# Performance work log

Measured on AMD Instinct MI355X. Metric: run time of the kernel, lower is better.

## Reference

```python
import jax, jax.numpy as jnp
import numpy as np

N, E, FIN, NH, FOUT = 50000, 800000, 128, 4, 16


def setup_inputs() -> dict:
    key = jax.random.key(0)
    ks = jax.random.split(key, 6)
    x = jax.random.normal(ks[0], (N, FIN), dtype=jnp.float32)
    edge_index = jax.random.randint(ks[1], (2, E), 0, N, dtype=jnp.int64)
    w_proj = jax.random.normal(ks[2], (NH * FOUT, FIN), dtype=jnp.float32) * 0.05
    a_src = jax.random.normal(ks[3], (NH, FOUT), dtype=jnp.float32) * 0.1
    a_trg = jax.random.normal(ks[4], (NH, FOUT), dtype=jnp.float32) * 0.1
    w_skip = jax.random.normal(ks[5], (NH * FOUT, FIN), dtype=jnp.float32) * 0.05
    return {"x": x, "edge_index": edge_index, "w_proj": w_proj,
            "a_src": a_src, "a_trg": a_trg, "w_skip": w_skip}


def reference(x, edge_index, w_proj, a_src, a_trg, w_skip):
    # Dropout is identity in eval mode.
    src, trg = edge_index[0], edge_index[1]
    # Project: [N, NH, FOUT]
    proj = (x @ w_proj.T).reshape(N, NH, FOUT)
    # Per-node attention logits: [N, NH]
    s_src = jnp.einsum('nhf,hf->nh', proj, a_src)
    s_trg = jnp.einsum('nhf,hf->nh', proj, a_trg)
    # Lift to edges and score: [E, NH]
    scores = jax.nn.leaky_relu(s_src[src] + s_trg[trg], negative_slope=0.2)
    # Global-max-shifted exp (matches original, which subtracts the global max)
    exp_scores = jnp.exp(scores - jnp.max(scores))
    # Segment-wise softmax denominator over target nodes
    denom = jax.ops.segment_sum(exp_scores, trg, num_segments=N)  # [N, NH]
    attn = exp_scores / (denom[trg] + 1e-16)                      # [E, NH]
    # Weighted aggregation of lifted source features: [N, NH, FOUT]
    weighted = proj[src] * attn[:, :, None]
    agg = jax.ops.segment_sum(weighted, trg, num_segments=N)
    # Skip projection (FOUT != FIN branch) and concat over heads
    out = agg + (x @ w_skip.T).reshape(N, NH, FOUT)
    out = out.reshape(N, NH * FOUT)
    return jax.nn.elu(out)
```

## Files before the change

kernel.cpp:

```cpp
#include <hip/hip_runtime.h>
#include <cstddef>

#define N_NODES 50000
#define N_EDGES 800000
#define FIN     128
#define NH      4
#define FOUT    16
#define COUT    64
#define STRIPS  (N_NODES / 16)
#define SCAN_BLOCKS ((N_NODES + 255) / 256)
#define NB      128
#define CHUNK   (N_EDGES / NB)
#define HW4     (N_NODES / 4)
#define HBYTES  (HW4 * 4)
#define NQ      4
#define BPQ     (NB / NQ)
#define PBLK    ((HW4 + 255) / 256)
#define E4      (N_EDGES / 4)
#define E4B     ((E4 + 255) / 256)

typedef __bf16 bf16x8 __attribute__((ext_vector_type(8)));
typedef float  f32x4  __attribute__((ext_vector_type(4)));

__global__ __launch_bounds__(256) void k0_init(
    const float* __restrict__ wproj, const float* __restrict__ wskip,
    __bf16* __restrict__ wb)
{
    int gid = blockIdx.x * 256 + threadIdx.x;
    if (gid < (128 * FIN) / 4) {
        int row = gid >> 5;
        float4 v = (row < 64) ? reinterpret_cast<const float4*>(wproj)[gid]
                              : reinterpret_cast<const float4*>(wskip)[gid - 2048];
        __bf16* o = wb + (size_t)gid * 4;
        o[0] = (__bf16)v.x; o[1] = (__bf16)v.y;
        o[2] = (__bf16)v.z; o[3] = (__bf16)v.w;
    }
}

__global__ __launch_bounds__(256) void k1_mfma(
    const float* __restrict__ x, const __bf16* __restrict__ wb,
    const float* __restrict__ asrc, const float* __restrict__ atrg,
    __bf16* __restrict__ projb, float* __restrict__ ssrc, float* __restrict__ strg,
    float* __restrict__ outv)
{
    const int lane  = threadIdx.x & 63;
    const int wid   = blockIdx.x * 4 + (threadIdx.x >> 6);
    const int strip = wid >> 1;
    const int half  = wid & 1;
    if (strip >= STRIPS) return;
    const int r = lane & 15;
    const int g = lane >> 4;
    const int row0 = strip * 16;

    bf16x8 bfr[4][4];
    #pragma unroll
    for (int j = 0; j < 4; ++j) {
        const __bf16* wrow = wb + (size_t)(half * 64 + j * 16 + r) * FIN;
        #pragma unroll
        for (int kk = 0; kk < 4; ++kk)
            bfr[j][kk] = *reinterpret_cast<const bf16x8*>(wrow + kk * 32 + g * 8);
    }

    const float* xrow = x + (size_t)(row0 + r) * FIN + g * 8;
    bf16x8 afr[4];
    #pragma unroll
    for (int kk = 0; kk < 4; ++kk) {
        float4 u0 = *reinterpret_cast<const float4*>(xrow + kk * 32);
        float4 u1 = *reinterpret_cast<const float4*>(xrow + kk * 32 + 4);
        bf16x8 a;
        a[0] = (__bf16)u0.x; a[1] = (__bf16)u0.y;
        a[2] = (__bf16)u0.z; a[3] = (__bf16)u0.w;
        a[4] = (__bf16)u1.x; a[5] = (__bf16)u1.y;
        a[6] = (__bf16)u1.z; a[7] = (__bf16)u1.w;
        afr[kk] = a;
    }

    f32x4 acc[4] = {{0.f,0.f,0.f,0.f},{0.f,0.f,0.f,0.f},
                    {0.f,0.f,0.f,0.f},{0.f,0.f,0.f,0.f}};
    #pragma unroll
    for (int kk = 0; kk < 4; ++kk)
        #pragma unroll
        for (int j = 0; j < 4; ++j)
            acc[j] = __builtin_amdgcn_mfma_f32_16x16x32_bf16(
                         afr[kk], bfr[j][kk], acc[j], 0, 0, 0);

    if (!half) {
        #pragma unroll
        for (int j = 0; j < 4; ++j)
            #pragma unroll
            for (int q = 0; q < 4; ++q)
                projb[(size_t)(row0 + g * 4 + q) * COUT + j * 16 + r] =
                    (__bf16)acc[j][q];
        #pragma unroll
        for (int j = 0; j < 4; ++j) {
            const float as = asrc[j * 16 + r];
            const float at = atrg[j * 16 + r];
            #pragma unroll
            for (int q = 0; q < 4; ++q) {
                float ts = acc[j][q] * as;
                float tt = acc[j][q] * at;
                ts += __shfl_xor(ts, 1); ts += __shfl_xor(ts, 2);
                ts += __shfl_xor(ts, 4); ts += __shfl_xor(ts, 8);
                tt += __shfl_xor(tt, 1); tt += __shfl_xor(tt, 2);
                tt += __shfl_xor(tt, 4); tt += __shfl_xor(tt, 8);
                if (r == 0) {
                    int n = row0 + g * 4 + q;
                    ssrc[(size_t)n * NH + j] = ts;
                    strg[(size_t)n * NH + j] = tt;
                }
            }
        }
    } else {
        #pragma unroll
        for (int j = 0; j < 4; ++j)
            #pragma unroll
            for (int q = 0; q < 4; ++q)
                outv[(size_t)(row0 + g * 4 + q) * COUT + j * 16 + r] = acc[j][q];
    }
}

__global__ __launch_bounds__(1024) void k_hist(
    const int* __restrict__ ei, unsigned* __restrict__ histG,
    unsigned char* __restrict__ rank)
{
    extern __shared__ unsigned h[];
    const int t = threadIdx.x;
    for (int i = t; i < HW4; i += 1024) h[i] = 0;
    __syncthreads();
    const int base = blockIdx.x * CHUNK;
    for (int i = t; i < CHUNK; i += 1024) {
        int tg = ei[N_EDGES + base + i];
        int sh = (tg & 3) * 8;
        unsigned old = atomicAdd(&h[tg >> 2], 1u << sh);
        rank[base + i] = (unsigned char)((old >> sh) & 0xffu);
    }
    __syncthreads();
    unsigned* out = histG + (size_t)blockIdx.x * HW4;
    for (int i = t; i < HW4; i += 1024) out[i] = h[i];
}

__global__ __launch_bounds__(256) void k_colscanA(
    const unsigned* __restrict__ histG, unsigned* __restrict__ offG,
    unsigned* __restrict__ partial)
{
    int p = blockIdx.x * 256 + threadIdx.x;
    if (p >= HW4) return;
    int q = blockIdx.y;
    unsigned run = 0;
    #pragma unroll 4
    for (int b = q * BPQ; b < (q + 1) * BPQ; ++b) {
        unsigned v = histG[(size_t)b * HW4 + p];
        offG[(size_t)b * HW4 + p] = run;
        run += v;
    }
    partial[(size_t)q * HW4 + p] = run;
}

__global__ __launch_bounds__(256) void k_scanfuse(
    const unsigned* __restrict__ partial, unsigned* __restrict__ baseQ,
    int* __restrict__ deg, int* __restrict__ tmpExc, int* __restrict__ bsum)
{
    __shared__ int sm[256];
    const int t = threadIdx.x;
    if (t < 64) {
        int p = blockIdx.x * 64 + t;
        if (p < HW4) {
            unsigned s = 0;
            #pragma unroll
            for (int q = 0; q < NQ; ++q) {
                baseQ[(size_t)q * HW4 + p] = s;
                s += partial[(size_t)q * HW4 + p];
            }
            int4 d4 = make_int4((int)(s & 0xffu), (int)((s >> 8) & 0xffu),
                                (int)((s >> 16) & 0xffu), (int)(s >> 24));
            reinterpret_cast<int4*>(deg)[p] = d4;
            sm[4 * t + 0] = d4.x; sm[4 * t + 1] = d4.y;
            sm[4 * t + 2] = d4.z; sm[4 * t + 3] = d4.w;
        } else {
            sm[4 * t + 0] = 0; sm[4 * t + 1] = 0;
            sm[4 * t + 2] = 0; sm[4 * t + 3] = 0;
        }
    }
    __syncthreads();
    int v = sm[t];
    #pragma unroll
    for (int off = 1; off < 256; off <<= 1) {
        int x = (t >= off) ? sm[t - off] : 0;
        __syncthreads();
        sm[t] += x;
        __syncthreads();
    }
    int i = blockIdx.x * 256 + t;
    if (i < N_NODES) tmpExc[i] = sm[t] - v;
    if (t == 255) bsum[blockIdx.x] = sm[t];
}

__global__ __launch_bounds__(256) void scan_b(
    const int* __restrict__ bsum, int* __restrict__ bOff)
{
    __shared__ int sm[256];
    int t = threadIdx.x;
    int v = (t < SCAN_BLOCKS) ? bsum[t] : 0;
    sm[t] = v; __syncthreads();
    #pragma unroll
    for (int off = 1; off < 256; off <<= 1) {
        int x = (t >= off) ? sm[t - off] : 0;
        __syncthreads();
        sm[t] += x;
        __syncthreads();
    }
    if (t < SCAN_BLOCKS) bOff[t] = sm[t] - v;
}

__global__ __launch_bounds__(256) void k_scatter(
    const int* __restrict__ ei, const unsigned char* __restrict__ rank,
    const unsigned* __restrict__ offG, const unsigned* __restrict__ baseQ,
    const int* __restrict__ tmpExc, const int* __restrict__ bOff,
    int* __restrict__ srcs)
{
    int e4 = blockIdx.x * 256 + threadIdx.x;
    if (e4 >= E4) return;
    int4 s4 = reinterpret_cast<const int4*>(ei)[e4];
    int4 t4 = reinterpret_cast<const int4*>(ei + N_EDGES)[e4];
    uchar4 r4 = reinterpret_cast<const uchar4*>(rank)[e4];
    const int e0 = e4 * 4;
    int ss[4] = {s4.x, s4.y, s4.z, s4.w};
    int tt[4] = {t4.x, t4.y, t4.z, t4.w};
    int rr[4] = {r4.x, r4.y, r4.z, r4.w};
    #pragma unroll
    for (int u = 0; u < 4; ++u) {
        int tg = tt[u];
        int b  = (e0 + u) / CHUNK;
        int sh = (tg & 3) * 8;
        unsigned cw = offG[(size_t)b * HW4 + (tg >> 2)]
                    + baseQ[(size_t)(b / BPQ) * HW4 + (tg >> 2)];
        int cross = (int)((cw >> sh) & 0xffu);
        int slot  = tmpExc[tg] + bOff[tg >> 8] + cross + rr[u];
        srcs[slot] = ss[u];
    }
}

__global__ __launch_bounds__(256) void k3_gather(
    const int* __restrict__ tmpExc, const int* __restrict__ bOff,
    const int* __restrict__ deg, const int* __restrict__ srcs,
    const float* __restrict__ ssrc, const float* __restrict__ strg,
    const __bf16* __restrict__ projb, float* __restrict__ outv)
{
    const int lane = threadIdx.x & 63;
    const int node = __builtin_amdgcn_readfirstlane(blockIdx.x * 4 + (threadIdx.x >> 6));
    if (node >= N_NODES) return;
    const int h = lane >> 4;
    const int begin = tmpExc[node] + bOff[node >> 8];
    const int dg    = deg[node];
    const float st  = strg[(size_t)node * NH + h];
    const float skip = outv[(size_t)node * COUT + lane];

    float acc = 0.f, dsum = 0.f;
    int i = 0;
    for (; i + 8 <= dg; i += 8) {
        int s[8]; float a[8], p[8];
        #pragma unroll
        for (int u = 0; u < 8; ++u) s[u] = srcs[begin + i + u];
        #pragma unroll
        for (int u = 0; u < 8; ++u) a[u] = ssrc[(size_t)s[u] * NH + h];
        #pragma unroll
        for (int u = 0; u < 8; ++u) p[u] = (float)projb[(size_t)s[u] * COUT + lane];
        #pragma unroll
        for (int u = 0; u < 8; ++u) {
            float z = a[u] + st;
            z = (z >= 0.f) ? z : 0.2f * z;
            float ez = __expf(z);
            dsum += ez;
            acc += ez * p[u];
        }
    }
    for (; i + 4 <= dg; i += 4) {
        int s[4]; float a[4], p[4];
        #pragma unroll
        for (int u = 0; u < 4; ++u) s[u] = srcs[begin + i + u];
        #pragma unroll
        for (int u = 0; u < 4; ++u) a[u] = ssrc[(size_t)s[u] * NH + h];
        #pragma unroll
        for (int u = 0; u < 4; ++u) p[u] = (float)projb[(size_t)s[u] * COUT + lane];
        #pragma unroll
        for (int u = 0; u < 4; ++u) {
            float z = a[u] + st;
            z = (z >= 0.f) ? z : 0.2f * z;
            float ez = __expf(z);
            dsum += ez;
            acc += ez * p[u];
        }
    }
    for (; i < dg; ++i) {
        int s = srcs[begin + i];
        float z = ssrc[(size_t)s * NH + h] + st;
        z = (z >= 0.f) ? z : 0.2f * z;
        float ez = __expf(z);
        float p  = (float)projb[(size_t)s * COUT + lane];
        dsum += ez;
        acc += ez * p;
    }
    float o = acc / (dsum + 1e-16f) + skip;
    o = (o > 0.f) ? o : expm1f(o);
    outv[(size_t)node * COUT + lane] = o;
}

extern "C" void kernel_launch(void* const* d_in, const int* in_sizes, int n_in,
                              void* d_out, int out_size, void* d_ws, size_t ws_size,
                              hipStream_t stream)
{
    const float* x     = (const float*)d_in[0];
    const int*   ei    = (const int*)  d_in[1];
    const float* wproj = (const float*)d_in[2];
    const float* asrc  = (const float*)d_in[3];
    const float* atrg  = (const float*)d_in[4];
    const float* wskip = (const float*)d_in[5];
    float* outv = (float*)d_out;

    __bf16* projb = (__bf16*)d_ws;
    float* base  = (float*)d_ws;
    float* ssrc  = base + (size_t)N_NODES * COUT;
    float* strg  = ssrc + (size_t)N_NODES * NH;
    int* deg     = (int*)(strg + (size_t)N_NODES * NH);
    int* tmpExc  = deg    + N_NODES;
    int* bsum    = tmpExc + N_NODES;
    int* bOff    = bsum   + 256;
    int* srcs    = bOff   + 256;
    unsigned* histG   = (unsigned*)(srcs + N_EDGES);
    unsigned* offG    = histG + (size_t)NB * HW4;
    unsigned* partial = offG  + (size_t)NB * HW4;
    unsigned* baseQ   = partial + (size_t)NQ * HW4;
    unsigned char* rank = (unsigned char*)(baseQ + (size_t)NQ * HW4);
    __bf16* wb   = (__bf16*)(rank + N_EDGES);

    k0_init<<<16, 256, 0, stream>>>(wproj, wskip, wb);

    int k1_blocks = (STRIPS * 2 + 3) / 4;
    k1_mfma<<<k1_blocks, 256, 0, stream>>>(x, wb, asrc, atrg,
                                           projb, ssrc, strg, outv);

    k_hist<<<NB, 1024, HBYTES, stream>>>(ei, histG, rank);

    k_colscanA<<<dim3(PBLK, NQ), 256, 0, stream>>>(histG, offG, partial);

    k_scanfuse<<<SCAN_BLOCKS, 256, 0, stream>>>(partial, baseQ, deg,
                                                tmpExc, bsum);
    scan_b<<<1, 256, 0, stream>>>(bsum, bOff);

    k_scatter<<<E4B, 256, 0, stream>>>(ei, rank, offG, baseQ,
                                       tmpExc, bOff, srcs);

    int k3_blocks = (N_NODES + 3) / 4;
    k3_gather<<<k3_blocks, 256, 0, stream>>>(tmpExc, bOff, deg, srcs,
                                             ssrc, strg, projb, outv);
}
```

Before: 99.29 us.

## Process two row strips per MFMA wave and split node edges across two waves

Measured after the change: 114.8 us. +15.6%, slower.

```diff
diff --git a/kernel.cpp b/kernel.cpp
--- a/kernel.cpp
+++ b/kernel.cpp
@@ -8,6 +8,7 @@
 #define FOUT    16
 #define COUT    64
 #define STRIPS  (N_NODES / 16)
+#define PAIRS   ((STRIPS + 1) / 2)
 #define SCAN_BLOCKS ((N_NODES + 255) / 256)
 #define NB      128
 #define CHUNK   (N_EDGES / NB)
@@ -43,14 +44,14 @@
     __bf16* __restrict__ projb, float* __restrict__ ssrc, float* __restrict__ strg,
     float* __restrict__ outv)
 {
-    const int lane  = threadIdx.x & 63;
-    const int wid   = blockIdx.x * 4 + (threadIdx.x >> 6);
-    const int strip = wid >> 1;
-    const int half  = wid & 1;
-    if (strip >= STRIPS) return;
+    const int lane = threadIdx.x & 63;
+    const int wid  = blockIdx.x * 4 + (threadIdx.x >> 6);
+    const int pair = wid >> 1;
+    const int half = wid & 1;
+    if (pair >= PAIRS) return;
     const int r = lane & 15;
     const int g = lane >> 4;
-    const int row0 = strip * 16;
+    const int row0 = pair * 32;
 
     bf16x8 bfr[4][4];
     #pragma unroll
@@ -61,52 +62,80 @@
             bfr[j][kk] = *reinterpret_cast<const bf16x8*>(wrow + kk * 32 + g * 8);
     }
 
-    const float* xrow = x + (size_t)(row0 + r) * FIN + g * 8;
-    bf16x8 afr[4];
+    const int rowA0 = row0 + r;
+    int rowA1 = row0 + 16 + r;
+    if (rowA1 >= N_NODES) rowA1 = N_NODES - 1;
+    const float* xr0 = x + (size_t)rowA0 * FIN + g * 8;
+    const float* xr1 = x + (size_t)rowA1 * FIN + g * 8;
+    bf16x8 af0[4], af1[4];
     #pragma unroll
     for (int kk = 0; kk < 4; ++kk) {
-        float4 u0 = *reinterpret_cast<const float4*>(xrow + kk * 32);
-        float4 u1 = *reinterpret_cast<const float4*>(xrow + kk * 32 + 4);
-        bf16x8 a;
+        float4 u0 = *reinterpret_cast<const float4*>(xr0 + kk * 32);
+        float4 u1 = *reinterpret_cast<const float4*>(xr0 + kk * 32 + 4);
+        float4 v0 = *reinterpret_cast<const float4*>(xr1 + kk * 32);
+        float4 v1 = *reinterpret_cast<const float4*>(xr1 + kk * 32 + 4);
+        bf16x8 a, b;
         a[0] = (__bf16)u0.x; a[1] = (__bf16)u0.y;
         a[2] = (__bf16)u0.z; a[3] = (__bf16)u0.w;
         a[4] = (__bf16)u1.x; a[5] = (__bf16)u1.y;
         a[6] = (__bf16)u1.z; a[7] = (__bf16)u1.w;
-        afr[kk] = a;
-    }
-
-    f32x4 acc[4] = {{0.f,0.f,0.f,0.f},{0.f,0.f,0.f,0.f},
-                    {0.f,0.f,0.f,0.f},{0.f,0.f,0.f,0.f}};
+        b[0] = (__bf16)v0.x; b[1] = (__bf16)v0.y;
+        b[2] = (__bf16)v0.z; b[3] = (__bf16)v0.w;
+        b[4] = (__bf16)v1.x; b[5] = (__bf16)v1.y;
+        b[6] = (__bf16)v1.z; b[7] = (__bf16)v1.w;
+        af0[kk] = a; af1[kk] = b;
+    }
+
+    f32x4 acc0[4] = {{0.f,0.f,0.f,0.f},{0.f,0.f,0.f,0.f},
+                     {0.f,0.f,0.f,0.f},{0.f,0.f,0.f,0.f}};
+    f32x4 acc1[4] = {{0.f,0.f,0.f,0.f},{0.f,0.f,0.f,0.f},
+                     {0.f,0.f,0.f,0.f},{0.f,0.f,0.f,0.f}};
     #pragma unroll
     for (int kk = 0; kk < 4; ++kk)
         #pragma unroll
-        for (int j = 0; j < 4; ++j)
-            acc[j] = __builtin_amdgcn_mfma_f32_16x16x32_bf16(
-                         afr[kk], bfr[j][kk], acc[j], 0, 0, 0);
+        for (int j = 0; j < 4; ++j) {
+            acc0[j] = __builtin_amdgcn_mfma_f32_16x16x32_bf16(
+                          af0[kk], bfr[j][kk], acc0[j], 0, 0, 0);
+            acc1[j] = __builtin_amdgcn_mfma_f32_16x16x32_bf16(
+                          af1[kk], bfr[j][kk], acc1[j], 0, 0, 0);
+        }
 
     if (!half) {
         #pragma unroll
         for (int j = 0; j < 4; ++j)
             #pragma unroll
-            for (int q = 0; q < 4; ++q)
-                projb[(size_t)(row0 + g * 4 + q) * COUT + j * 16 + r] =
-                    (__bf16)acc[j][q];
+            for (int q = 0; q < 4; ++q) {
+                int n0 = row0 + g * 4 + q;
+                int n1 = n0 + 16;
+                projb[(size_t)n0 * COUT + j * 16 + r] = (__bf16)acc0[j][q];
+                if (n1 < N_NODES)
+                    projb[(size_t)n1 * COUT + j * 16 + r] = (__bf16)acc1[j][q];
+            }
         #pragma unroll
         for (int j = 0; j < 4; ++j) {
             const float as = asrc[j * 16 + r];
             const float at = atrg[j * 16 + r];
             #pragma unroll
             for (int q = 0; q < 4; ++q) {
-                float ts = acc[j][q] * as;
-                float tt = acc[j][q] * at;
-                ts += __shfl_xor(ts, 1); ts += __shfl_xor(ts, 2);
-                ts += __shfl_xor(ts, 4); ts += __shfl_xor(ts, 8);
-                tt += __shfl_xor(tt, 1); tt += __shfl_xor(tt, 2);
-                tt += __shfl_xor(tt, 4); tt += __shfl_xor(tt, 8);
+                float ts0 = acc0[j][q] * as, tt0 = acc0[j][q] * at;
+                float ts1 = acc1[j][q] * as, tt1 = acc1[j][q] * at;
+                ts0 += __shfl_xor(ts0, 1); ts0 += __shfl_xor(ts0, 2);
+                ts0 += __shfl_xor(ts0, 4); ts0 += __shfl_xor(ts0, 8);
+                tt0 += __shfl_xor(tt0, 1); tt0 += __shfl_xor(tt0, 2);
+                tt0 += __shfl_xor(tt0, 4); tt0 += __shfl_xor(tt0, 8);
+                ts1 += __shfl_xor(ts1, 1); ts1 += __shfl_xor(ts1, 2);
+                ts1 += __shfl_xor(ts1, 4); ts1 += __shfl_xor(ts1, 8);
+                tt1 += __shfl_xor(tt1, 1); tt1 += __shfl_xor(tt1, 2);
+                tt1 += __shfl_xor(tt1, 4); tt1 += __shfl_xor(tt1, 8);
                 if (r == 0) {
-                    int n = row0 + g * 4 + q;
-                    ssrc[(size_t)n * NH + j] = ts;
-                    strg[(size_t)n * NH + j] = tt;
+                    int n0 = row0 + g * 4 + q;
+                    int n1 = n0 + 16;
+                    ssrc[(size_t)n0 * NH + j] = ts0;
+                    strg[(size_t)n0 * NH + j] = tt0;
+                    if (n1 < N_NODES) {
+                        ssrc[(size_t)n1 * NH + j] = ts1;
+                        strg[(size_t)n1 * NH + j] = tt1;
+                    }
                 }
             }
         }
@@ -114,8 +143,13 @@
         #pragma unroll
         for (int j = 0; j < 4; ++j)
             #pragma unroll
-            for (int q = 0; q < 4; ++q)
-                outv[(size_t)(row0 + g * 4 + q) * COUT + j * 16 + r] = acc[j][q];
+            for (int q = 0; q < 4; ++q) {
+                int n0 = row0 + g * 4 + q;
+                int n1 = n0 + 16;
+                outv[(size_t)n0 * COUT + j * 16 + r] = acc0[j][q];
+                if (n1 < N_NODES)
+                    outv[(size_t)n1 * COUT + j * 16 + r] = acc1[j][q];
+            }
     }
 }
 
@@ -246,21 +280,27 @@
     const float* __restrict__ ssrc, const float* __restrict__ strg,
     const __bf16* __restrict__ projb, float* __restrict__ outv)
 {
+    __shared__ float redA[2][2][64];
+    __shared__ float redD[2][2][64];
     const int lane = threadIdx.x & 63;
-    const int node = __builtin_amdgcn_readfirstlane(blockIdx.x * 4 + (threadIdx.x >> 6));
-    if (node >= N_NODES) return;
+    const int ns   = threadIdx.x >> 7;
+    const int sub  = (threadIdx.x >> 6) & 1;
+    const int node = __builtin_amdgcn_readfirstlane(blockIdx.x * 2 + ns);
     const int h = lane >> 4;
     const int begin = tmpExc[node] + bOff[node >> 8];
     const int dg    = deg[node];
+    const int h0    = (dg + 1) >> 1;
+    const int myBeg = begin + (sub ? h0 : 0);
+    const int myCnt = sub ? (dg - h0) : h0;
     const float st  = strg[(size_t)node * NH + h];
-    const float skip = outv[(size_t)node * COUT + lane];
+    const float skip = (sub == 0) ? outv[(size_t)node * COUT + lane] : 0.f;
 
     float acc = 0.f, dsum = 0.f;
     int i = 0;
-    for (; i + 8 <= dg; i += 8) {
+    for (; i + 8 <= myCnt; i += 8) {
         int s[8]; float a[8], p[8];
         #pragma unroll
-        for (int u = 0; u < 8; ++u) s[u] = srcs[begin + i + u];
+        for (int u = 0; u < 8; ++u) s[u] = srcs[myBeg + i + u];
         #pragma unroll
         for (int u = 0; u < 8; ++u) a[u] = ssrc[(size_t)s[u] * NH + h];
         #pragma unroll
@@ -274,10 +314,10 @@
             acc += ez * p[u];
         }
     }
-    for (; i + 4 <= dg; i += 4) {
+    for (; i + 4 <= myCnt; i += 4) {
         int s[4]; float a[4], p[4];
         #pragma unroll
-        for (int u = 0; u < 4; ++u) s[u] = srcs[begin + i + u];
+        for (int u = 0; u < 4; ++u) s[u] = srcs[myBeg + i + u];
         #pragma unroll
         for (int u = 0; u < 4; ++u) a[u] = ssrc[(size_t)s[u] * NH + h];
         #pragma unroll
@@ -291,8 +331,8 @@
             acc += ez * p[u];
         }
     }
-    for (; i < dg; ++i) {
-        int s = srcs[begin + i];
+    for (; i < myCnt; ++i) {
+        int s = srcs[myBeg + i];
         float z = ssrc[(size_t)s * NH + h] + st;
         z = (z >= 0.f) ? z : 0.2f * z;
         float ez = __expf(z);
@@ -300,9 +340,17 @@
         dsum += ez;
         acc += ez * p;
     }
-    float o = acc / (dsum + 1e-16f) + skip;
-    o = (o > 0.f) ? o : expm1f(o);
-    outv[(size_t)node * COUT + lane] = o;
+
+    redA[ns][sub][lane] = acc;
+    redD[ns][sub][lane] = dsum;
+    __syncthreads();
+    if (sub == 0) {
+        float accT = redA[ns][0][lane] + redA[ns][1][lane];
+        float dsT  = redD[ns][0][lane] + redD[ns][1][lane];
+        float o = accT / (dsT + 1e-16f) + skip;
+        o = (o > 0.f) ? o : expm1f(o);
+        outv[(size_t)node * COUT + lane] = o;
+    }
 }
 
 extern "C" void kernel_launch(void* const* d_in, const int* in_sizes, int n_in,
@@ -335,7 +383,7 @@
 
     k0_init<<<16, 256, 0, stream>>>(wproj, wskip, wb);
 
-    int k1_blocks = (STRIPS * 2 + 3) / 4;
+    int k1_blocks = (PAIRS * 2 + 3) / 4;
     k1_mfma<<<k1_blocks, 256, 0, stream>>>(x, wb, asrc, atrg,
                                            projb, ssrc, strg, outv);
 
@@ -350,7 +398,7 @@
     k_scatter<<<E4B, 256, 0, stream>>>(ei, rank, offG, baseQ,
                                        tmpExc, bOff, srcs);
 
-    int k3_blocks = (N_NODES + 3) / 4;
+    int k3_blocks = N_NODES / 2;
     k3_gather<<<k3_blocks, 256, 0, stream>>>(tmpExc, bOff, deg, srcs,
                                              ssrc, strg, projb, outv);
 }
```
